# Kernel tuning notes

Hardware: AMD Instinct MI355X
Metric: run time of the kernel (lower is better)

## Reference

```python
import jax, jax.numpy as jnp
import numpy as np

CDIM = 32
SCALES = (1, 16, 64, 256, 1024, 4096)  # last entry == T
INV_TEMP = 100.0
ENT_W = 0.1
COMMIT_W = 0.2
Q_SCALE = 1.0 / float(np.sqrt(CDIM))


def _interp_area(x, pt):
    # x: [B, T, C] -> [B, pt, C]; T divisible by pt so 'area' == block mean
    B, T, C = x.shape
    return x.reshape(B, pt, T // pt, C).mean(axis=2)


def _interp_linear(x, T):
    # x: [B, pt, C] -> [B, T, C]; mode='linear', align_corners=False
    pt = x.shape[1]
    pos = (jnp.arange(T, dtype=jnp.float32) + 0.5) * (pt / T) - 0.5
    pos = jnp.clip(pos, 0.0, pt - 1.0)
    lo = jnp.floor(pos).astype(jnp.int32)
    hi = jnp.minimum(lo + 1, pt - 1)
    w = (pos - lo.astype(jnp.float32))[None, :, None]
    return x[:, lo] * (1.0 - w) + x[:, hi] * w


def _bsq(f):
    # L2 normalize (torch F.normalize: clamp_min on norm)
    f = f / jnp.maximum(jnp.linalg.norm(f, axis=-1, keepdims=True), 1e-12)
    # sign quantize with STE
    zhat = jnp.where(f > 0, Q_SCALE, -Q_SCALE).astype(f.dtype)
    quantized = f + jax.lax.stop_gradient(zhat - f)
    # soft entropy loss
    p = jax.nn.sigmoid(-4.0 * f * (INV_TEMP / float(np.sqrt(CDIM))))
    prob = jnp.stack([p, 1.0 - p], axis=-1)  # [B, T, C, 2]
    ent = lambda c: -(c * jnp.log(c + 1e-8)).sum(axis=-1)
    per_sample_entropy = ent(prob).sum(axis=-1).mean()
    avg_prob = prob.mean(axis=(0, 1))  # [C, 2]
    cb_entropy = ent(avg_prob).sum()
    entropy_penalty = (per_sample_entropy - cb_entropy) / INV_TEMP
    commit = ((jax.lax.stop_gradient(quantized) - f) ** 2).sum(axis=-1).mean()
    aux = entropy_penalty * ENT_W + commit * COMMIT_W
    bits = (quantized > 0).astype(jnp.int32)
    return quantized, bits, aux


def setup_inputs() -> dict:
    key = jax.random.key(0)
    B, T, C = 128, SCALES[-1], CDIM
    return {"f_BTC": jax.random.normal(key, (B, T, C), dtype=jnp.float32)}


def reference(f_BTC):
    B, T, C = f_BTC.shape
    quantized_out = jnp.zeros_like(f_BTC)
    residual = f_BTC
    losses, bit_list = [], []
    for pt in SCALES:
        interp_res = _interp_area(residual, pt) if pt != T else residual
        q, bits, loss = _bsq(interp_res)
        q = _interp_linear(q, T) if pt != T else q
        residual = residual - jax.lax.stop_gradient(q)
        quantized_out = quantized_out + q
        bit_list.append(bits)
        losses.append(loss)
    all_losses = jnp.stack(losses, axis=-1)       # [num_scales]
    all_bits = jnp.concatenate(bit_list, axis=1)  # [B, sum(SCALES), C]
    return quantized_out, all_bits, all_losses
```

## Files before the change

kernel.cpp:

```cpp
#include <hip/hip_runtime.h>
#include <hip/hip_bf16.h>
#include <cstddef>
#include <cstdint>

#define NB 128
#define NT 4096
#define NC 32
#define BITROWS 5457
#define QV_ROWS 1361
#define QOUT_ELEMS (NB*NT*NC)
#define BITS_ELEMS (NB*BITROWS*NC)

#define ACC_OFF  22298624
#define S16_OFF  22302720

__device__ __constant__ float kQSC = 0.17677669529663687f;
__device__ __constant__ float kSIG = 17.67766952966369f;

__device__ __forceinline__ float interp_slice(const float* __restrict__ q, int P, int base, int t, int c) {
  float pos = ((float)t + 0.5f) * ((float)P * (1.0f / 4096.0f)) - 0.5f;
  pos = fminf(fmaxf(pos, 0.0f), (float)(P - 1));
  const int lo = (int)pos;
  const int hi = min(lo + 1, P - 1);
  const float w = pos - (float)lo;
  const float a = __fmul_rn(q[(lo - base) * NC + c], 1.0f - w);
  const float b = __fmul_rn(q[(hi - base) * NC + c], w);
  return __fadd_rn(a, b);
}

__device__ __forceinline__ void process_elem(
    float msum, float invn, int b, int rowOff, int j, int c,
    float* qlsRow, float* __restrict__ qvG, float* __restrict__ bitsG,
    float& entA, float& comA, float& pA)
{
  const float m = msum * invn;
  float ss = m * m;
  #pragma unroll
  for (int mk = 16; mk; mk >>= 1) ss += __shfl_xor(ss, mk, 32);
  const float den = fmaxf(sqrtf(ss), 1e-12f);
  const float fn = m / den;
  const bool bit = fn > 0.0f;
  const float zh = bit ? kQSC : -kQSC;
  const float qvv = fn + (zh - fn);
  if (qlsRow) qlsRow[c] = qvv;
  if (qvG) qvG[(size_t)b * (QV_ROWS * NC) + (size_t)(rowOff + j) * NC + c] = qvv;
  bitsG[(size_t)b * (BITROWS * NC) + (size_t)(rowOff + j) * NC + c] = bit ? 1.0f : 0.0f;
  const float arg = (-4.0f * fn) * kSIG;
  const float p = 1.0f / (1.0f + __expf(-arg));
  const float ent = -(p * __logf(p + 1e-8f) + (1.0f - p) * __logf((1.0f - p) + 1e-8f));
  const float d = qvv - fn;
  entA += ent; comA += d * d; pA += p;
}

__device__ __forceinline__ float quant_silent(float msum, float invn) {
  const float m = msum * invn;
  float ss = m * m;
  #pragma unroll
  for (int mk = 16; mk; mk >>= 1) ss += __shfl_xor(ss, mk, 32);
  const float den = fmaxf(sqrtf(ss), 1e-12f);
  const float fn = m / den;
  const float zh = (fn > 0.0f) ? kQSC : -kQSC;
  return fn + (zh - fn);
}

__device__ __forceinline__ void reduce_losses(
    int sIdx, float entA, float comA, float pA, int tid, int nWaves,
    double* __restrict__ acc, float* redE, float* redC, float* redP)
{
  float e = entA, cm = comA;
  #pragma unroll
  for (int mk = 32; mk; mk >>= 1) { e += __shfl_xor(e, mk, 64); cm += __shfl_xor(cm, mk, 64); }
  const float p = pA + __shfl_xor(pA, 32, 64);
  const int w = tid >> 6, lane = tid & 63;
  if (lane == 0) { redE[w] = e; redC[w] = cm; }
  if (lane < 32) redP[w * 32 + lane] = p;
  __syncthreads();
  if (tid == 0) {
    double te = 0.0, tc = 0.0;
    for (int i = 0; i < nWaves; ++i) { te += (double)redE[i]; tc += (double)redC[i]; }
    atomicAdd(&acc[sIdx], te);
    atomicAdd(&acc[6 + sIdx], tc);
  }
  if (tid < 32) {
    float tp = 0.0f;
    for (int i = 0; i < nWaves; ++i) tp += redP[i * 32 + tid];
    atomicAdd(&acc[12 + sIdx * 32 + tid], (double)tp);
  }
  __syncthreads();
}

__global__ __launch_bounds__(256) void k_sum16(const float* __restrict__ f, float* __restrict__ S16) {
  const int idx = blockIdx.x * 256 + threadIdx.x;
  if (idx >= NB * 256 * NC) return;
  const int c = idx & 31;
  const int j = (idx >> 5) & 255;
  const int b = idx >> 13;
  const float* p = f + (size_t)b * (NT * NC) + (size_t)j * 16 * NC + c;
  float s = 0.0f;
  #pragma unroll
  for (int k = 0; k < 16; ++k) s += p[k * NC];
  S16[idx] = s;
}

__global__ __launch_bounds__(1024) void k_s0(
    const float* __restrict__ S16g, float* __restrict__ qv,
    float* __restrict__ bitsOut, double* __restrict__ acc)
{
  __shared__ float red[1024];
  __shared__ float redE[16], redC[16], redP[16 * 32];
  const int b = blockIdx.x, tid = threadIdx.x, c = tid & 31;
  const float* __restrict__ sb = S16g + (size_t)b * 8192;
  {
    const int g = tid >> 5;
    float part = 0.0f;
    #pragma unroll
    for (int j = 0; j < 8; ++j) part += sb[(size_t)(g * 8 + j) * NC + c];
    red[tid] = part;
  }
  __syncthreads();
  float entA = 0.0f, comA = 0.0f, pA = 0.0f;
  if (tid < 32) {
    float msum = 0.0f;
    for (int g = 0; g < 32; ++g) msum += red[g * 32 + tid];
    process_elem(msum, 1.0f / 4096.0f, b, 0, 0, tid, nullptr, qv, bitsOut, entA, comA, pA);
  }
  reduce_losses(0, entA, comA, pA, tid, 16, acc, redE, redC, redP);
}

__global__ __launch_bounds__(1024) void k_coarse4(
    const float* __restrict__ S16g,
    float* __restrict__ qv, float* __restrict__ bitsOut, double* __restrict__ acc)
{
  __shared__ float S[96 * NC];
  __shared__ float q1s[6 * NC];
  __shared__ float q2s[18 * NC];
  __shared__ float redE[16], redC[16], redP[16 * 32];
  const int b = blockIdx.x >> 2, seg = blockIdx.x & 3;
  const int tid = threadIdx.x, c = tid & 31;
  const int s0r = 64 * seg - 16;
  const int base1 = 4 * seg - 1, base2 = 16 * seg - 1;
  const float* __restrict__ sb = S16g + (size_t)b * 8192;
  const float* __restrict__ qb = qv + (size_t)b * (QV_ROWS * NC);

  const float corr = 16.0f * qb[c];
  for (int e = tid; e < 96 * NC; e += 1024) {
    const int rw = min(max(s0r + (e >> 5), 0), 255);
    S[e] = sb[(size_t)rw * NC + (e & 31)] - corr;
  }
  __syncthreads();

  float ent, com, pp;

  ent = com = pp = 0.0f;
  if (tid < 6 * NC) {
    const int r = tid >> 5, j = base1 + r;
    if (j >= 0 && j < 16) {
      float msum = 0.0f;
      for (int jj = 0; jj < 16; ++jj) msum += S[(j * 16 + jj - s0r) * NC + c];
      if (r >= 1 && r <= 4)
        process_elem(msum, 1.0f / 256.0f, b, 1, j, c, &q1s[r * NC], qv, bitsOut, ent, com, pp);
      else
        q1s[r * NC + c] = quant_silent(msum, 1.0f / 256.0f);
    }
  }
  reduce_losses(1, ent, com, pp, tid, 16, acc, redE, redC, redP);

  for (int e = tid; e < 72 * NC; e += 1024) {
    const int g = 64 * seg - 4 + (e >> 5);
    if (g >= 0 && g < 256) {
      float cs = 0.0f;
      #pragma unroll
      for (int k = 0; k < 16; ++k) cs += interp_slice(q1s, 16, base1, g * 16 + k, c);
      S[(g - s0r) * NC + c] -= cs;
    }
  }
  __syncthreads();

  ent = com = pp = 0.0f;
  if (tid < 18 * NC) {
    const int r = tid >> 5, j2 = base2 + r;
    if (j2 >= 0 && j2 < 64) {
      float msum = 0.0f;
      #pragma unroll
      for (int jj = 0; jj < 4; ++jj) msum += S[(j2 * 4 + jj - s0r) * NC + c];
      if (r >= 1 && r <= 16)
        process_elem(msum, 1.0f / 64.0f, b, 17, j2, c, &q2s[r * NC], qv, bitsOut, ent, com, pp);
      else
        q2s[r * NC + c] = quant_silent(msum, 1.0f / 64.0f);
    }
  }
  reduce_losses(2, ent, com, pp, tid, 16, acc, redE, redC, redP);

  for (int e = tid; e < 64 * NC; e += 1024) {
    const int g = 64 * seg + (e >> 5);
    float cs = 0.0f;
    #pragma unroll
    for (int k = 0; k < 16; ++k) cs += interp_slice(q2s, 64, base2, g * 16 + k, c);
    S[(g - s0r) * NC + c] -= cs;
  }
  __syncthreads();

  ent = com = pp = 0.0f;
  for (int out = tid; out < 64 * NC; out += 1024) {
    const int g = 64 * seg + (out >> 5);
    process_elem(S[(g - s0r) * NC + c], 1.0f / 16.0f, b, 81, g, c, nullptr, qv, bitsOut, ent, com, pp);
  }
  reduce_losses(3, ent, com, pp, tid, 16, acc, redE, redC, redP);
}

__global__ __launch_bounds__(256) void k_s45(
    const float* __restrict__ f, const float* __restrict__ qv,
    float* __restrict__ qout, float* __restrict__ bitsOut, double* __restrict__ acc)
{
  __shared__ float ql0[NC];
  __shared__ float ql1[3 * NC];
  __shared__ float ql2[6 * NC];
  __shared__ float ql3[18 * NC];
  __shared__ float ql4[66 * NC];
  __shared__ float redE[4], redC[4], redP[4 * 32];
  const int b = blockIdx.x >> 4, seg = blockIdx.x & 15;
  const int tid = threadIdx.x, c = tid & 31, rloc = tid >> 5;
  const float* __restrict__ qb = qv + (size_t)b * (QV_ROWS * NC);
  const float* __restrict__ fb = f + (size_t)b * (NT * NC);
  const int b1 = seg - 1, b2 = 4 * seg - 1, b3 = 16 * seg - 1, b4 = 64 * seg - 1;
  if (tid < NC) ql0[tid] = qb[tid];
  for (int e = tid; e < 3 * NC; e += 256) {
    const int r = min(max(b1 + (e >> 5), 0), 15);
    ql1[e] = qb[(1 + r) * NC + (e & 31)];
  }
  for (int e = tid; e < 6 * NC; e += 256) {
    const int r = min(max(b2 + (e >> 5), 0), 63);
    ql2[e] = qb[(17 + r) * NC + (e & 31)];
  }
  for (int e = tid; e < 18 * NC; e += 256) {
    const int r = min(max(b3 + (e >> 5), 0), 255);
    ql3[e] = qb[(81 + r) * NC + (e & 31)];
  }
  __syncthreads();

  float entA4 = 0.0f, comA4 = 0.0f, pA4 = 0.0f;
  float entB = 0.0f, comB = 0.0f, pB = 0.0f;

  auto do_A = [&](int p, float rc[4], float qc[4]) {
    const int i = seg * 64 + p * 8 + rloc;
    const float* fp = fb + (size_t)i * 4 * NC + c;
    float msum = 0.0f;
    #pragma unroll
    for (int k = 0; k < 4; ++k) {
      const int t = i * 4 + k;
      const float q0 = ql0[c];
      const float q1 = interp_slice(ql1, 16,  b1, t, c);
      const float q2 = interp_slice(ql2, 64,  b2, t, c);
      const float q3 = interp_slice(ql3, 256, b3, t, c);
      float r = fp[k * NC];
      r -= q0; r -= q1; r -= q2; r -= q3;
      float qs = q0; qs += q1; qs += q2; qs += q3;
      rc[k] = r; qc[k] = qs;
      msum += r;
    }
    process_elem(msum, 0.25f, b, 337, i, c,
                 &ql4[(size_t)(i - b4) * NC], nullptr, bitsOut, entA4, comA4, pA4);
  };

  auto do_halo = [&](int hr) {
    const float* fp = fb + (size_t)hr * 4 * NC + c;
    float msum = 0.0f;
    #pragma unroll
    for (int k = 0; k < 4; ++k) {
      const int t = hr * 4 + k;
      float r = fp[k * NC];
      r -= ql0[c];
      r -= interp_slice(ql1, 16,  b1, t, c);
      r -= interp_slice(ql2, 64,  b2, t, c);
      r -= interp_slice(ql3, 256, b3, t, c);
      msum += r;
    }
    ql4[(size_t)(hr - b4) * NC + c] = quant_silent(msum, 0.25f);
  };

  auto do_B = [&](int p, const float rc[4], const float qc[4]) {
    const int i = seg * 64 + p * 8 + rloc;
    #pragma unroll
    for (int k = 0; k < 4; ++k) {
      const int t = i * 4 + k;
      const float q4 = interp_slice(ql4, 1024, b4, t, c);
      float r = rc[k];
      r -= q4;
      float qs = qc[k];
      qs += q4;
      float ss = r * r;
      #pragma unroll
      for (int mk = 16; mk; mk >>= 1) ss += __shfl_xor(ss, mk, 32);
      const float den = fmaxf(sqrtf(ss), 1e-12f);
      const float fn = r / den;
      const bool bit = fn > 0.0f;
      const float zh = bit ? kQSC : -kQSC;
      const float qvv = fn + (zh - fn);
      qout[(size_t)b * (NT * NC) + (size_t)t * NC + c] = qs + qvv;
      bitsOut[(size_t)b * (BITROWS * NC) + (size_t)(1361 + t) * NC + c] = bit ? 1.0f : 0.0f;
      const float arg = (-4.0f * fn) * kSIG;
      const float p2 = 1.0f / (1.0f + __expf(-arg));
      entB += -(p2 * __logf(p2 + 1e-8f) + (1.0f - p2) * __logf((1.0f - p2) + 1e-8f));
      const float d = qvv - fn;
      comB += d * d;
      pB += p2;
    }
  };

  float rAp[4], qsAp[4];
  float rAc[4], qsAc[4];

  do_A(0, rAp, qsAp);
  if (rloc == 0 && seg > 0) do_halo(64 * seg - 1);

  for (int p = 1; p < 8; ++p) {
    do_A(p, rAc, qsAc);
    __syncthreads();
    do_B(p - 1, rAp, qsAp);
    #pragma unroll
    for (int k = 0; k < 4; ++k) { rAp[k] = rAc[k]; qsAp[k] = qsAc[k]; }
  }
  if (rloc == 1 && seg < 15) do_halo(64 * seg + 64);
  __syncthreads();
  do_B(7, rAp, qsAp);

  reduce_losses(4, entA4, comA4, pA4, tid, 4, acc, redE, redC, redP);
  reduce_losses(5, entB, comB, pB, tid, 4, acc, redE, redC, redP);
}

__global__ void k_losses(const double* __restrict__ acc, float* __restrict__ out) {
  const int s = threadIdx.x;
  if (s >= 6) return;
  const int pts[6] = {1, 16, 64, 256, 1024, 4096};
  const double n = 128.0 * (double)pts[s];
  const double pse = acc[s] / n;
  const double commit = acc[6 + s] / n;
  double cbe = 0.0;
  for (int c = 0; c < 32; ++c) {
    const double ap = acc[12 + s * 32 + c] / n;
    cbe += -(ap * log(ap + 1e-8) + (1.0 - ap) * log((1.0 - ap) + 1e-8));
  }
  const double pen = (pse - cbe) / 100.0;
  out[s] = (float)(pen * 0.1 + commit * 0.2);
}

extern "C" void kernel_launch(void* const* d_in, const int* in_sizes, int n_in,
                              void* d_out, int out_size, void* d_ws, size_t ws_size,
                              hipStream_t stream) {
  const float* f = (const float*)d_in[0];
  float* qout = (float*)d_out;
  float* bitsOut = qout + QOUT_ELEMS;
  float* lossesOut = qout + (QOUT_ELEMS + BITS_ELEMS);
  float* qv = (float*)d_ws;
  double* acc = (double*)((char*)d_ws + ACC_OFF);
  float* S16 = (float*)((char*)d_ws + S16_OFF);

  hipMemsetAsync(acc, 0, 204 * sizeof(double), stream);
  k_sum16<<<4096, 256, 0, stream>>>(f, S16);
  k_s0<<<NB, 1024, 0, stream>>>(S16, qv, bitsOut, acc);
  k_coarse4<<<NB * 4, 1024, 0, stream>>>(S16, qv, bitsOut, acc);
  k_s45<<<NB * 16, 256, 0, stream>>>(f, qv, qout, bitsOut, acc);
  k_losses<<<1, 64, 0, stream>>>(acc, lossesOut);
}
```

Measured before the change: 320.6 us.

## Fuse 16-row block sums into k_s0 and precompute interpolation indices in k_s45

Removes the separate k_sum16 launch: k_s0 now reads the input directly, writes the S16 partial sums and reduces them in the same pass, with only 128 blocks of 1024 threads. In k_s45 the per-element linear-interpolation position, clamp and index math is replaced by per-row precomputed lo/hi pointers and incremental weights, including special-cased edges. This cuts one launch and a pass over the input, but the fused sum runs on far fewer blocks, which may limit bandwidth, and the hand-derived weights must match the reference rounding exactly.

```diff
diff --git a/kernel.cpp b/kernel.cpp
--- a/kernel.cpp
+++ b/kernel.cpp
@@ -25,6 +25,12 @@
   const float w = pos - (float)lo;
   const float a = __fmul_rn(q[(lo - base) * NC + c], 1.0f - w);
   const float b = __fmul_rn(q[(hi - base) * NC + c], w);
+  return __fadd_rn(a, b);
+}
+
+__device__ __forceinline__ float interp_w(const float* __restrict__ plo, const float* __restrict__ phi, float w) {
+  const float a = __fmul_rn(*plo, 1.0f - w);
+  const float b = __fmul_rn(*phi, w);
   return __fadd_rn(a, b);
 }
 
@@ -89,39 +95,32 @@
   __syncthreads();
 }
 
-__global__ __launch_bounds__(256) void k_sum16(const float* __restrict__ f, float* __restrict__ S16) {
-  const int idx = blockIdx.x * 256 + threadIdx.x;
-  if (idx >= NB * 256 * NC) return;
-  const int c = idx & 31;
-  const int j = (idx >> 5) & 255;
-  const int b = idx >> 13;
-  const float* p = f + (size_t)b * (NT * NC) + (size_t)j * 16 * NC + c;
-  float s = 0.0f;
-  #pragma unroll
-  for (int k = 0; k < 16; ++k) s += p[k * NC];
-  S16[idx] = s;
-}
-
 __global__ __launch_bounds__(1024) void k_s0(
-    const float* __restrict__ S16g, float* __restrict__ qv,
-    float* __restrict__ bitsOut, double* __restrict__ acc)
+    const float* __restrict__ f, float* __restrict__ S16,
+    float* __restrict__ qv, float* __restrict__ bitsOut, double* __restrict__ acc)
 {
   __shared__ float red[1024];
   __shared__ float redE[16], redC[16], redP[16 * 32];
   const int b = blockIdx.x, tid = threadIdx.x, c = tid & 31;
-  const float* __restrict__ sb = S16g + (size_t)b * 8192;
-  {
-    const int g = tid >> 5;
-    float part = 0.0f;
-    #pragma unroll
-    for (int j = 0; j < 8; ++j) part += sb[(size_t)(g * 8 + j) * NC + c];
-    red[tid] = part;
-  }
+  const int g = tid >> 5;
+  const float* __restrict__ fbase = f + (size_t)b * (NT * NC);
+  float part = 0.0f;
+  #pragma unroll
+  for (int j = 0; j < 8; ++j) {
+    const int row = g * 8 + j;
+    const float* p = fbase + (size_t)row * 16 * NC + c;
+    float s = 0.0f;
+    #pragma unroll
+    for (int k = 0; k < 16; ++k) s += p[k * NC];
+    S16[(size_t)b * 8192 + (size_t)row * NC + c] = s;
+    part += s;
+  }
+  red[tid] = part;
   __syncthreads();
   float entA = 0.0f, comA = 0.0f, pA = 0.0f;
   if (tid < 32) {
     float msum = 0.0f;
-    for (int g = 0; g < 32; ++g) msum += red[g * 32 + tid];
+    for (int gg = 0; gg < 32; ++gg) msum += red[gg * 32 + tid];
     process_elem(msum, 1.0f / 4096.0f, b, 0, 0, tid, nullptr, qv, bitsOut, entA, comA, pA);
   }
   reduce_losses(0, entA, comA, pA, tid, 16, acc, redE, redC, redP);
@@ -213,9 +212,9 @@
     float* __restrict__ qout, float* __restrict__ bitsOut, double* __restrict__ acc)
 {
   __shared__ float ql0[NC];
-  __shared__ float ql1[3 * NC];
-  __shared__ float ql2[6 * NC];
-  __shared__ float ql3[18 * NC];
+  __shared__ float q1s[3 * NC];
+  __shared__ float q2s[6 * NC];
+  __shared__ float q3s[18 * NC];
   __shared__ float ql4[66 * NC];
   __shared__ float redE[4], redC[4], redP[4 * 32];
   const int b = blockIdx.x >> 4, seg = blockIdx.x & 15;
@@ -226,15 +225,15 @@
   if (tid < NC) ql0[tid] = qb[tid];
   for (int e = tid; e < 3 * NC; e += 256) {
     const int r = min(max(b1 + (e >> 5), 0), 15);
-    ql1[e] = qb[(1 + r) * NC + (e & 31)];
+    q1s[e] = qb[(1 + r) * NC + (e & 31)];
   }
   for (int e = tid; e < 6 * NC; e += 256) {
     const int r = min(max(b2 + (e >> 5), 0), 63);
-    ql2[e] = qb[(17 + r) * NC + (e & 31)];
+    q2s[e] = qb[(17 + r) * NC + (e & 31)];
   }
   for (int e = tid; e < 18 * NC; e += 256) {
     const int r = min(max(b3 + (e >> 5), 0), 255);
-    ql3[e] = qb[(81 + r) * NC + (e & 31)];
+    q3s[e] = qb[(81 + r) * NC + (e & 31)];
   }
   __syncthreads();
 
@@ -244,14 +243,53 @@
   auto do_A = [&](int p, float rc[4], float qc[4]) {
     const int i = seg * 64 + p * 8 + rloc;
     const float* fp = fb + (size_t)i * 4 * NC + c;
+
+    const bool lh1 = (i & 63) < 32;
+    int rl1 = lh1 ? 0 : 1, rh1;
+    float wb1 = __fmaf_rn((float)((i & 63) << 2), 0.00390625f,
+                          lh1 ? 0.501953125f : -0.498046875f);
+    {
+      const bool cz = (seg == 0) && lh1, ch = (seg == 15) && !lh1;
+      if (cz) rl1 = 1;
+      rh1 = ch ? rl1 : rl1 + 1;
+      if (cz || ch) wb1 = -4.0f;
+    }
+    const int a2r = (i >> 4) & 3;
+    const bool lh2 = (i & 15) < 8;
+    int rl2 = a2r + (lh2 ? 0 : 1), rh2;
+    float wb2 = __fmaf_rn((float)((i & 15) << 2), 0.015625f,
+                          lh2 ? 0.5078125f : -0.4921875f);
+    {
+      const bool cz = (seg == 0) && (a2r == 0) && lh2, ch = (seg == 15) && (a2r == 3) && !lh2;
+      if (cz) rl2 = 1;
+      rh2 = ch ? rl2 : rl2 + 1;
+      if (cz || ch) wb2 = -4.0f;
+    }
+    const int a3r = (i >> 2) & 15;
+    const bool lh3 = (i & 3) < 2;
+    int rl3 = a3r + (lh3 ? 0 : 1), rh3;
+    float wb3 = __fmaf_rn((float)((i & 3) << 2), 0.0625f,
+                          lh3 ? 0.53125f : -0.46875f);
+    {
+      const bool cz = (seg == 0) && (a3r == 0) && lh3, ch = (seg == 15) && (a3r == 15) && !lh3;
+      if (cz) rl3 = 1;
+      rh3 = ch ? rl3 : rl3 + 1;
+      if (cz || ch) wb3 = -4.0f;
+    }
+    const float* p1lo = &q1s[rl1 * NC + c]; const float* p1hi = &q1s[rh1 * NC + c];
+    const float* p2lo = &q2s[rl2 * NC + c]; const float* p2hi = &q2s[rh2 * NC + c];
+    const float* p3lo = &q3s[rl3 * NC + c]; const float* p3hi = &q3s[rh3 * NC + c];
+    const float q0 = ql0[c];
+
     float msum = 0.0f;
     #pragma unroll
     for (int k = 0; k < 4; ++k) {
-      const int t = i * 4 + k;
-      const float q0 = ql0[c];
-      const float q1 = interp_slice(ql1, 16,  b1, t, c);
-      const float q2 = interp_slice(ql2, 64,  b2, t, c);
-      const float q3 = interp_slice(ql3, 256, b3, t, c);
+      float w1 = wb1 + (float)k * 0.00390625f; w1 = (w1 < 0.0f) ? 0.0f : w1;
+      float w2 = wb2 + (float)k * 0.015625f;   w2 = (w2 < 0.0f) ? 0.0f : w2;
+      float w3 = wb3 + (float)k * 0.0625f;     w3 = (w3 < 0.0f) ? 0.0f : w3;
+      const float q1 = interp_w(p1lo, p1hi, w1);
+      const float q2 = interp_w(p2lo, p2hi, w2);
+      const float q3 = interp_w(p3lo, p3hi, w3);
       float r = fp[k * NC];
       r -= q0; r -= q1; r -= q2; r -= q3;
       float qs = q0; qs += q1; qs += q2; qs += q3;
@@ -270,9 +308,9 @@
       const int t = hr * 4 + k;
       float r = fp[k * NC];
       r -= ql0[c];
-      r -= interp_slice(ql1, 16,  b1, t, c);
-      r -= interp_slice(ql2, 64,  b2, t, c);
-      r -= interp_slice(ql3, 256, b3, t, c);
+      r -= interp_slice(q1s, 16,  b1, t, c);
+      r -= interp_slice(q2s, 64,  b2, t, c);
+      r -= interp_slice(q3s, 256, b3, t, c);
       msum += r;
     }
     ql4[(size_t)(hr - b4) * NC + c] = quant_silent(msum, 0.25f);
@@ -280,14 +318,27 @@
 
   auto do_B = [&](int p, const float rc[4], const float qc[4]) {
     const int i = seg * 64 + p * 8 + rloc;
+    const int ir = p * 8 + rloc;
+    const float* r0 = &ql4[(size_t)ir * NC + c];
+    const float* r1 = &ql4[(size_t)(ir + 1) * NC + c];
+    const float* r2 = &ql4[(size_t)(ir + 2) * NC + c];
+    const bool e0 = (i == 0), e1 = (i == 1023);
     #pragma unroll
     for (int k = 0; k < 4; ++k) {
-      const int t = i * 4 + k;
-      const float q4 = interp_slice(ql4, 1024, b4, t, c);
+      const float* plo; const float* phi; float w4;
+      if (k < 2) {
+        plo = e0 ? r1 : r0; phi = e0 ? r2 : r1;
+        w4 = e0 ? 0.0f : (k == 0 ? 0.625f : 0.875f);
+      } else {
+        plo = r1; phi = e1 ? r1 : r2;
+        w4 = e1 ? 0.0f : (k == 2 ? 0.125f : 0.375f);
+      }
+      const float q4 = interp_w(plo, phi, w4);
       float r = rc[k];
       r -= q4;
       float qs = qc[k];
       qs += q4;
+      const int t = i * 4 + k;
       float ss = r * r;
       #pragma unroll
       for (int mk = 16; mk; mk >>= 1) ss += __shfl_xor(ss, mk, 32);
@@ -356,8 +407,7 @@
   float* S16 = (float*)((char*)d_ws + S16_OFF);
 
   hipMemsetAsync(acc, 0, 204 * sizeof(double), stream);
-  k_sum16<<<4096, 256, 0, stream>>>(f, S16);
-  k_s0<<<NB, 1024, 0, stream>>>(S16, qv, bitsOut, acc);
+  k_s0<<<NB, 1024, 0, stream>>>(f, S16, qv, bitsOut, acc);
   k_coarse4<<<NB * 4, 1024, 0, stream>>>(S16, qv, bitsOut, acc);
   k_s45<<<NB * 16, 256, 0, stream>>>(f, qv, qout, bitsOut, acc);
   k_losses<<<1, 64, 0, stream>>>(acc, lossesOut);
```

Result: no change. 318.2 us, median of 2 (-0.8%).
